# Kernel optimization log

Hardware: AMD Instinct MI355X
Metric: run time of the kernel (lower is better)

Reference implementation:

```python
import jax, jax.numpy as jnp
import numpy as np

B, D, K = 65536, 256, 10
LOG_2PI = float(np.log(2.0 * np.pi))


def setup_inputs() -> dict:
    key = jax.random.key(0)
    k1, k2 = jax.random.split(key)
    q_z = jax.random.normal(k1, (B, D), dtype=jnp.float32)
    # Xavier-uniform init for mu lookup (approximated with normal scale)
    mu_table = jax.random.normal(k2, (K, D), dtype=jnp.float32) * 0.1
    # logvar lookup initialized to log(exp(0)**2) = 0
    logvar_table = jnp.zeros((K, D), dtype=jnp.float32)
    return {"q_z": q_z, "mu_table": mu_table, "logvar_table": logvar_table}


def reference(q_z, mu_table, logvar_table):
    # q_z: [B, D]; mu_table, logvar_table: [K, D]
    k = mu_table.shape[0]
    diff = q_z[:, None, :] - mu_table[None, :, :]              # [B, K, D]
    llh = -0.5 * (diff * diff / jnp.exp(logvar_table)[None]
                  + logvar_table[None] + LOG_2PI)              # [B, K, D]
    log_q_y_logit = jnp.sum(llh, axis=2) + jnp.log(1.0 / k)    # [B, K]
    q_y = jax.nn.softmax(log_q_y_logit, axis=1)                # [B, K]
    ind = jnp.argmax(q_y, axis=1)                              # [B]
    return (log_q_y_logit, q_y, ind)
```

## Files before the change

kernel.cpp:

```cpp
#include <hip/hip_runtime.h>
#include <hip/hip_bf16.h>
#include <math.h>

#define BB 65536
#define DD 256
#define KK 10
#define LOG_2PI 1.8378770664093453f
#define ROWS_PB 128
#define NCHUNK 4

__global__ __launch_bounds__(DD) void gmvae_prep(
    const float* __restrict__ mu_table,
    const float* __restrict__ logvar_table,
    float* __restrict__ tab,
    float* __restrict__ C)
{
    const int k = blockIdx.x;
    const int d = threadIdx.x;
    const float lv = logvar_table[k * DD + d];
    const float m  = mu_table[k * DD + d];
    const float iv = expf(-lv);
    const float a  = m * iv;

    const int c  = d >> 6;
    const int j  = (d >> 2) & 15;
    const int cc = d & 3;
    const int base = ((c * 16 + j) * KK + k) * 8 + cc;
    tab[base]     = iv;
    tab[base + 4] = -2.0f * a;

    float p = fmaf(m, a, lv);
    __shared__ float red[4];
    #pragma unroll
    for (int off = 32; off > 0; off >>= 1)
        p += __shfl_down(p, off, 64);
    if ((threadIdx.x & 63) == 0)
        red[threadIdx.x >> 6] = p;
    __syncthreads();
    if (threadIdx.x == 0) {
        const float s2 = (red[0] + red[1]) + (red[2] + red[3]);
        C[k] = -0.5f * (s2 + 256.0f * LOG_2PI) + logf(0.1f);
    }
}

__global__ __launch_bounds__(ROWS_PB) void gmvae_partial(
    const float* __restrict__ q_z,
    const float* __restrict__ tab,
    float* __restrict__ part)
{
    __shared__ float4 lds4[ROWS_PB * 9];
    const int tid  = threadIdx.x;
    const int blk  = blockIdx.x;
    const int c    = blk & 3;
    const int row0 = (blk >> 2) * ROWS_PB;

    const float4* __restrict__ q4 = reinterpret_cast<const float4*>(q_z);

    float acc[KK];
    #pragma unroll
    for (int k = 0; k < KK; ++k) acc[k] = 0.f;

    #pragma unroll
    for (int h = 0; h < 2; ++h) {
        if (h) __syncthreads();
        #pragma unroll
        for (int i = 0; i < 8; ++i) {
            const int flat = i * ROWS_PB + tid;
            const int rr = flat >> 3, f4 = flat & 7;
            lds4[rr * 9 + f4] =
                q4[(size_t)(row0 + rr) * 64 + c * 16 + h * 8 + f4];
        }
        __syncthreads();
        #pragma unroll
        for (int j = 0; j < 8; ++j) {
            const float4 q = lds4[tid * 9 + j];
            const float qx2 = q.x * q.x, qy2 = q.y * q.y;
            const float qz2 = q.z * q.z, qw2 = q.w * q.w;
            const float* tp = tab + (size_t)((c * 16 + h * 8 + j) * KK) * 8;
            #pragma unroll
            for (int k = 0; k < KK; ++k) {
                const float4 iv = *reinterpret_cast<const float4*>(tp + k * 8);
                const float4 na = *reinterpret_cast<const float4*>(tp + k * 8 + 4);
                acc[k] = fmaf(qx2, iv.x, acc[k]);
                acc[k] = fmaf(q.x, na.x, acc[k]);
                acc[k] = fmaf(qy2, iv.y, acc[k]);
                acc[k] = fmaf(q.y, na.y, acc[k]);
                acc[k] = fmaf(qz2, iv.z, acc[k]);
                acc[k] = fmaf(q.z, na.z, acc[k]);
                acc[k] = fmaf(qw2, iv.w, acc[k]);
                acc[k] = fmaf(q.w, na.w, acc[k]);
            }
        }
    }

    #pragma unroll
    for (int k = 0; k < KK; ++k)
        part[(size_t)(c * KK + k) * BB + row0 + tid] = acc[k];
}

__global__ __launch_bounds__(256) void gmvae_final(
    const float* __restrict__ part,
    const float* __restrict__ C,
    float* __restrict__ out)
{
    const int t   = blockIdx.x * 256 + threadIdx.x;
    const int c   = t & 3;
    const int row = t >> 2;

    float l[KK];
    #pragma unroll
    for (int k = 0; k < KK; ++k) {
        float v = part[(size_t)(c * KK + k) * BB + row];
        v += __shfl_xor(v, 1, 64);
        v += __shfl_xor(v, 2, 64);
        l[k] = fmaf(v, -0.5f, C[k]);
    }

    float mx = l[0];
    #pragma unroll
    for (int k = 1; k < KK; ++k) mx = fmaxf(mx, l[k]);

    float e[KK];
    float sum = 0.f;
    #pragma unroll
    for (int k = 0; k < KK; ++k) { e[k] = __expf(l[k] - mx); sum += e[k]; }
    const float inv = 1.0f / sum;

    int idx = 0;
    float best = l[0];
    #pragma unroll
    for (int k = 1; k < KK; ++k)
        if (l[k] > best) { best = l[k]; idx = k; }

    if (c == 0) {
        float2* __restrict__ o1 = reinterpret_cast<float2*>(out) + (size_t)row * 5;
        #pragma unroll
        for (int k = 0; k < 5; ++k)
            o1[k] = make_float2(l[2 * k], l[2 * k + 1]);
    } else if (c == 1) {
        float2* __restrict__ o2 =
            reinterpret_cast<float2*>(out + (size_t)BB * KK) + (size_t)row * 5;
        #pragma unroll
        for (int k = 0; k < 5; ++k)
            o2[k] = make_float2(e[2 * k] * inv, e[2 * k + 1] * inv);
    } else if (c == 2) {
        out[(size_t)2 * BB * KK + row] = (float)idx;
    }
}

extern "C" void kernel_launch(void* const* d_in, const int* in_sizes, int n_in,
                              void* d_out, int out_size, void* d_ws, size_t ws_size,
                              hipStream_t stream) {
    const float* q_z    = (const float*)d_in[0];
    const float* mu     = (const float*)d_in[1];
    const float* logvar = (const float*)d_in[2];
    float* out = (float*)d_out;

    float* tab  = (float*)d_ws;
    float* C    = tab + 5120;
    float* part = (float*)d_ws + 8192;

    gmvae_prep<<<KK, DD, 0, stream>>>(mu, logvar, tab, C);
    gmvae_partial<<<(BB / ROWS_PB) * NCHUNK, ROWS_PB, 0, stream>>>(q_z, tab, part);
    gmvae_final<<<(BB * 4) / 256, 256, 0, stream>>>(part, C, out);
}
```

Before: 110.5 us.

## Fuse partial-sum and softmax kernels with in-block LDS reduction over D chunks

Merges the partial-sum kernel and the final softmax/argmax kernel into one kernel. Each 256-thread block handles 64 rows, with four waves each covering a quarter of D. Partial sums are combined through LDS instead of a global partial buffer, which removes the write and re-read of that buffer and one launch. The table offset is made wave-uniform via readfirstlane so it can use scalar loads. The final stage runs on only one wave per block, leaving three waves idle during the epilogue.

```diff
diff --git a/kernel.cpp b/kernel.cpp
--- a/kernel.cpp
+++ b/kernel.cpp
@@ -6,8 +6,6 @@
 #define DD 256
 #define KK 10
 #define LOG_2PI 1.8378770664093453f
-#define ROWS_PB 128
-#define NCHUNK 4
 
 __global__ __launch_bounds__(DD) void gmvae_prep(
     const float* __restrict__ mu_table,
@@ -22,12 +20,10 @@
     const float iv = expf(-lv);
     const float a  = m * iv;
 
-    const int c  = d >> 6;
-    const int j  = (d >> 2) & 15;
-    const int cc = d & 3;
-    const int base = ((c * 16 + j) * KK + k) * 8 + cc;
-    tab[base]     = iv;
-    tab[base + 4] = -2.0f * a;
+    const int f    = d >> 2;
+    const int comp = d & 3;
+    tab[(f * KK + k) * 8 + comp]     = iv;
+    tab[(f * KK + k) * 8 + comp + 4] = -2.0f * a;
 
     float p = fmaf(m, a, lv);
     __shared__ float red[4];
@@ -43,16 +39,19 @@
     }
 }
 
-__global__ __launch_bounds__(ROWS_PB) void gmvae_partial(
+__global__ __launch_bounds__(256) void gmvae_main(
     const float* __restrict__ q_z,
     const float* __restrict__ tab,
-    float* __restrict__ part)
+    const float* __restrict__ C,
+    float* __restrict__ out)
 {
-    __shared__ float4 lds4[ROWS_PB * 9];
-    const int tid  = threadIdx.x;
-    const int blk  = blockIdx.x;
-    const int c    = blk & 3;
-    const int row0 = (blk >> 2) * ROWS_PB;
+    __shared__ float4 lds4[64 * 33];
+    float* comb = reinterpret_cast<float*>(lds4);
+
+    const int t    = threadIdx.x;
+    const int r    = t & 63;
+    const int c    = __builtin_amdgcn_readfirstlane(t >> 6);
+    const int row0 = blockIdx.x * 64;
 
     const float4* __restrict__ q4 = reinterpret_cast<const float4*>(q_z);
 
@@ -65,18 +64,20 @@
         if (h) __syncthreads();
         #pragma unroll
         for (int i = 0; i < 8; ++i) {
-            const int flat = i * ROWS_PB + tid;
-            const int rr = flat >> 3, f4 = flat & 7;
-            lds4[rr * 9 + f4] =
-                q4[(size_t)(row0 + rr) * 64 + c * 16 + h * 8 + f4];
+            const int flat = i * 256 + t;
+            const int rr = flat >> 5, ff = flat & 31;
+            lds4[rr * 33 + ff] = q4[(size_t)(row0 + rr) * 64 + h * 32 + ff];
         }
         __syncthreads();
+
         #pragma unroll
         for (int j = 0; j < 8; ++j) {
-            const float4 q = lds4[tid * 9 + j];
+            const float4 q = lds4[r * 33 + c * 8 + j];
             const float qx2 = q.x * q.x, qy2 = q.y * q.y;
             const float qz2 = q.z * q.z, qw2 = q.w * q.w;
-            const float* tp = tab + (size_t)((c * 16 + h * 8 + j) * KK) * 8;
+            const int toff = __builtin_amdgcn_readfirstlane(
+                ((h * 32 + c * 8 + j) * KK) * 8);
+            const float* tp = tab + toff;
             #pragma unroll
             for (int k = 0; k < KK; ++k) {
                 const float4 iv = *reinterpret_cast<const float4*>(tp + k * 8);
@@ -93,57 +94,48 @@
         }
     }
 
+    __syncthreads();
     #pragma unroll
     for (int k = 0; k < KK; ++k)
-        part[(size_t)(c * KK + k) * BB + row0 + tid] = acc[k];
-}
+        comb[t * 11 + k] = acc[k];
+    __syncthreads();
 
-__global__ __launch_bounds__(256) void gmvae_final(
-    const float* __restrict__ part,
-    const float* __restrict__ C,
-    float* __restrict__ out)
-{
-    const int t   = blockIdx.x * 256 + threadIdx.x;
-    const int c   = t & 3;
-    const int row = t >> 2;
+    if (t < 64) {
+        float l[KK];
+        #pragma unroll
+        for (int k = 0; k < KK; ++k) {
+            const float v = ((comb[(r)*11 + k]       + comb[(64 + r) * 11 + k]) +
+                             (comb[(128 + r) * 11 + k] + comb[(192 + r) * 11 + k]));
+            l[k] = fmaf(v, -0.5f, C[k]);
+        }
 
-    float l[KK];
-    #pragma unroll
-    for (int k = 0; k < KK; ++k) {
-        float v = part[(size_t)(c * KK + k) * BB + row];
-        v += __shfl_xor(v, 1, 64);
-        v += __shfl_xor(v, 2, 64);
-        l[k] = fmaf(v, -0.5f, C[k]);
-    }
+        float mx = l[0];
+        #pragma unroll
+        for (int k = 1; k < KK; ++k) mx = fmaxf(mx, l[k]);
 
-    float mx = l[0];
-    #pragma unroll
-    for (int k = 1; k < KK; ++k) mx = fmaxf(mx, l[k]);
+        float e[KK];
+        float sum = 0.f;
+        #pragma unroll
+        for (int k = 0; k < KK; ++k) { e[k] = __expf(l[k] - mx); sum += e[k]; }
+        const float inv = 1.0f / sum;
 
-    float e[KK];
-    float sum = 0.f;
-    #pragma unroll
-    for (int k = 0; k < KK; ++k) { e[k] = __expf(l[k] - mx); sum += e[k]; }
-    const float inv = 1.0f / sum;
+        int idx = 0;
+        float best = l[0];
+        #pragma unroll
+        for (int k = 1; k < KK; ++k)
+            if (l[k] > best) { best = l[k]; idx = k; }
 
-    int idx = 0;
-    float best = l[0];
-    #pragma unroll
-    for (int k = 1; k < KK; ++k)
-        if (l[k] > best) { best = l[k]; idx = k; }
-
-    if (c == 0) {
-        float2* __restrict__ o1 = reinterpret_cast<float2*>(out) + (size_t)row * 5;
-        #pragma unroll
-        for (int k = 0; k < 5; ++k)
-            o1[k] = make_float2(l[2 * k], l[2 * k + 1]);
-    } else if (c == 1) {
+        const int row = row0 + r;
+        float2* __restrict__ o1 =
+            reinterpret_cast<float2*>(out) + (size_t)row * 5;
         float2* __restrict__ o2 =
             reinterpret_cast<float2*>(out + (size_t)BB * KK) + (size_t)row * 5;
         #pragma unroll
         for (int k = 0; k < 5; ++k)
+            o1[k] = make_float2(l[2 * k], l[2 * k + 1]);
+        #pragma unroll
+        for (int k = 0; k < 5; ++k)
             o2[k] = make_float2(e[2 * k] * inv, e[2 * k + 1] * inv);
-    } else if (c == 2) {
         out[(size_t)2 * BB * KK + row] = (float)idx;
     }
 }
@@ -156,11 +148,9 @@
     const float* logvar = (const float*)d_in[2];
     float* out = (float*)d_out;
 
-    float* tab  = (float*)d_ws;
-    float* C    = tab + 5120;
-    float* part = (float*)d_ws + 8192;
+    float* tab = (float*)d_ws;
+    float* C   = tab + 5120;
 
     gmvae_prep<<<KK, DD, 0, stream>>>(mu, logvar, tab, C);
-    gmvae_partial<<<(BB / ROWS_PB) * NCHUNK, ROWS_PB, 0, stream>>>(q_z, tab, part);
-    gmvae_final<<<(BB * 4) / 256, 256, 0, stream>>>(part, C, out);
+    gmvae_main<<<BB / 64, 256, 0, stream>>>(q_z, tab, C, out);
 }
```

Result: no change. 108.9 us (-1.4%).
